# Optimization experiments

Hardware: AMD Instinct MI355X
Metric: run time of the kernel (lower is better)

Reference implementation:

```python
import jax, jax.numpy as jnp
import numpy as np

B, N, D, H, DK, DV, R = 4, 256, 256, 8, 32, 32, 64
EPS = 1e-6


def setup_inputs() -> dict:
    key = jax.random.key(0)
    ks = jax.random.split(key, 16)
    s = D ** -0.5
    return {
        "q": jax.random.normal(ks[0], (B, N, D), jnp.float32),
        "k": jax.random.normal(ks[1], (B, N, D), jnp.float32),
        "v": jax.random.normal(ks[2], (B, N, D), jnp.float32),
        "mask": jax.random.randint(ks[3], (B, N, N), 0, 2).astype(jnp.int32),
        "link": jax.random.uniform(ks[4], (B, N, N, R), jnp.float32),
        "Wq": jax.random.normal(ks[5], (D, H * DK), jnp.float32) * s,
        "Wk": jax.random.normal(ks[6], (D, H * DK), jnp.float32) * s,
        "Wr": jax.random.normal(ks[7], (D, H * DK), jnp.float32) * s,
        "Wv": jax.random.normal(ks[8], (D, H * DV), jnp.float32) * s,
        "Wvv": jax.random.normal(ks[9], (D, H * DV), jnp.float32) * s,
        "relationE": jax.random.normal(ks[10], (R, D), jnp.float32) * s,
        "Wo": jax.random.normal(ks[11], (H * DV, D), jnp.float32) * s,
        "gamma": jnp.ones((D,), jnp.float32),
        "beta": jnp.zeros((D,), jnp.float32),
    }


def reference(q, k, v, mask, link, Wq, Wk, Wr, Wv, Wvv, relationE, Wo, gamma, beta):
    # rela_num != 0 branch of Ruleformer MultiHeadAttention (dropout = identity, eval mode).
    residual = q
    b, n, d = q.shape
    # per-head projections of X (== q == residual in this branch): [b,h,n,dk]
    Xq = (q @ Wq).reshape(b, n, H, DK).transpose(0, 2, 1, 3)
    Xk = (q @ Wk).reshape(b, n, H, DK).transpose(0, 2, 1, 3)
    Xv = (q @ Wv).reshape(b, n, H, DV).transpose(0, 2, 1, 3)

    # calcE: relation-biased scores. Rk[b,i,j,h,d] = (link @ relationE @ Wr)
    Rk = jnp.einsum('bijr,re->bije', link, relationE @ Wr).reshape(b, n, n, H, DK)
    # attn[b,h,i,j] = Xq[b,h,i] . (Xk[b,h,j] + Rk[b,i,j,h])
    attn = jnp.einsum('bhid,bhjd->bhij', Xq, Xk)
    attn = attn + jnp.einsum('bijhd,bhid->bhij', Rk, Xq)
    attn = attn / (DK ** 0.5)
    attn = jnp.where(mask[:, None, :, :] == 0, -1e9, attn)
    alpha = jax.nn.softmax(attn, axis=-1)  # [b,h,n,n]

    # calcZ: Z[b,h,i] = sum_j alpha[b,h,i,j] * (Xv[b,h,j] + Rv[b,i,j,h])
    Rv = jnp.einsum('bijr,re->bije', link, relationE @ Wvv).reshape(b, n, n, H, DV)
    Z = jnp.einsum('bhij,bhjd->bhid', alpha, Xv)
    Z = Z + jnp.einsum('bhij,bijhd->bhid', alpha, Rv)

    out = Z.transpose(0, 2, 1, 3).reshape(b, n, H * DV) @ Wo
    out = out + residual
    mu = out.mean(-1, keepdims=True)
    var = ((out - mu) ** 2).mean(-1, keepdims=True)
    out = (out - mu) * jax.lax.rsqrt(var + EPS) * gamma + beta
    return out, alpha
```

## Files before the change

kernel.cpp:

```cpp
#include <hip/hip_runtime.h>
#include <math.h>

constexpr int B_ = 4, N_ = 256, D_ = 256, H_ = 8, DK_ = 32, DV_ = 32, R_ = 64;
constexpr float SCALE_ = 0.17677669529663687f;
constexpr float EPS_ = 1e-6f;

__global__ __launch_bounds__(256) void projekev_kernel(
        const float* __restrict__ q, const float* __restrict__ Wq,
        const float* __restrict__ Wk, const float* __restrict__ Wv,
        const float* __restrict__ relE, const float* __restrict__ Wr,
        const float* __restrict__ Wvv, float* __restrict__ Xq,
        float* __restrict__ Xk, float* __restrict__ Xv,
        float* __restrict__ Ek, float* __restrict__ Ev) {
    int blk = blockIdx.x;
    int t = threadIdx.x;
    __shared__ __align__(16) float ash[32 * 65];
    __shared__ __align__(16) float bsh[32 * 64];
    const float *src, *W;
    int rowbase, cbase, ct;
    float* dstE = nullptr;
    if (blk < 192) {
        ct = blk >> 4;
        int rt = blk & 15;
        src = q; rowbase = rt * 64;
        if (ct < 4)      { W = Wq; cbase = ct * 64; }
        else if (ct < 8) { W = Wk; cbase = (ct - 4) * 64; }
        else             { W = Wv; cbase = (ct - 8) * 64; }
    } else {
        int e = blk - 192;
        src = relE; rowbase = 0; ct = -1;
        W = (e < 4) ? Wr : Wvv;
        dstE = (e < 4) ? Ek : Ev;
        cbase = (e & 3) * 64;
    }
    int ti = t >> 4, tj = t & 15;
    float acc[4][4] = {{0.f}};
    for (int kc = 0; kc < 8; ++kc) {
        __syncthreads();
#pragma unroll
        for (int kk = 0; kk < 2; ++kk) {
            int m = t + kk * 256;
            int i = m >> 3, kq = m & 7;
            float4 v = *(const float4*)(src + (size_t)(rowbase + i) * 256 + kc * 32 + kq * 4);
            ash[(kq * 4 + 0) * 65 + i] = v.x;
            ash[(kq * 4 + 1) * 65 + i] = v.y;
            ash[(kq * 4 + 2) * 65 + i] = v.z;
            ash[(kq * 4 + 3) * 65 + i] = v.w;
        }
#pragma unroll
        for (int kk = 0; kk < 2; ++kk) {
            int m = t + kk * 256;
            int k = m >> 4, j4 = m & 15;
            float4 v = *(const float4*)(W + (size_t)(kc * 32 + k) * 256 + cbase + j4 * 4);
            *(float4*)(bsh + k * 64 + j4 * 4) = v;
        }
        __syncthreads();
#pragma unroll 8
        for (int k = 0; k < 32; ++k) {
            float4 av = *(const float4*)(ash + k * 65 + ti * 4);
            float4 bv = *(const float4*)(bsh + k * 64 + tj * 4);
            acc[0][0] += av.x * bv.x; acc[0][1] += av.x * bv.y;
            acc[0][2] += av.x * bv.z; acc[0][3] += av.x * bv.w;
            acc[1][0] += av.y * bv.x; acc[1][1] += av.y * bv.y;
            acc[1][2] += av.y * bv.z; acc[1][3] += av.y * bv.w;
            acc[2][0] += av.z * bv.x; acc[2][1] += av.z * bv.y;
            acc[2][2] += av.z * bv.z; acc[2][3] += av.z * bv.w;
            acc[3][0] += av.w * bv.x; acc[3][1] += av.w * bv.y;
            acc[3][2] += av.w * bv.z; acc[3][3] += av.w * bv.w;
        }
    }
    if (dstE) {
#pragma unroll
        for (int a = 0; a < 4; ++a) {
            int row = ti * 4 + a;
            *(float4*)(dstE + (size_t)row * 256 + cbase + tj * 4) =
                make_float4(acc[a][0], acc[a][1], acc[a][2], acc[a][3]);
        }
    } else {
        float* dst = (ct < 4) ? Xq : (ct < 8) ? Xk : Xv;
        int gcol = (ct & 3) * 64 + tj * 4;
        int h = gcol >> 5, dk = gcol & 31;
#pragma unroll
        for (int a = 0; a < 4; ++a) {
            int row = rowbase + ti * 4 + a;
            int bb = row >> 8, n = row & 255;
            *(float4*)(dst + ((size_t)(bb * 8 + h) * 256 + n) * 32 + dk) =
                make_float4(acc[a][0], acc[a][1], acc[a][2], acc[a][3]);
        }
    }
}

__global__ __launch_bounds__(256) void qkT_kernel(
        const float* __restrict__ Xq, const float* __restrict__ Xk,
        const float* __restrict__ Ek, float* __restrict__ qk,
        float* __restrict__ T) {
    int x = blockIdx.x;
    int t = threadIdx.x;
    __shared__ __align__(16) float xqsh[32 * 64];
    __shared__ __align__(16) float bsh2[32 * 64];
    bool isT = (x >= 512);
    int jt, it, bh;
    if (!isT) { jt = x & 3; it = (x >> 2) & 3; bh = x >> 4; }
    else      { int e = x - 512; jt = 0; it = e & 3; bh = e >> 2; }
    int b = bh >> 3, h = bh & 7;
#pragma unroll
    for (int k = 0; k < 2; ++k) {
        int m = t + k * 256;
        int i = m >> 3, dq4 = m & 7;
        float4 v = *(const float4*)(Xq + ((size_t)(bh * 256 + it * 64 + i)) * 32 + dq4 * 4);
        xqsh[(dq4 * 4 + 0) * 64 + i] = v.x;
        xqsh[(dq4 * 4 + 1) * 64 + i] = v.y;
        xqsh[(dq4 * 4 + 2) * 64 + i] = v.z;
        xqsh[(dq4 * 4 + 3) * 64 + i] = v.w;
    }
    if (!isT) {
#pragma unroll
        for (int k = 0; k < 2; ++k) {
            int m = t + k * 256;
            int i = m >> 3, dq4 = m & 7;
            float4 u = *(const float4*)(Xk + ((size_t)(bh * 256 + jt * 64 + i)) * 32 + dq4 * 4);
            bsh2[(dq4 * 4 + 0) * 64 + i] = u.x;
            bsh2[(dq4 * 4 + 1) * 64 + i] = u.y;
            bsh2[(dq4 * 4 + 2) * 64 + i] = u.z;
            bsh2[(dq4 * 4 + 3) * 64 + i] = u.w;
        }
    } else {
        int r = t >> 2, dq = t & 3;
#pragma unroll
        for (int kk = 0; kk < 2; ++kk) {
            int dq4 = dq + kk * 4;
            float4 v = *(const float4*)(Ek + r * 256 + h * 32 + dq4 * 4);
            bsh2[(dq4 * 4 + 0) * 64 + r] = v.x;
            bsh2[(dq4 * 4 + 1) * 64 + r] = v.y;
            bsh2[(dq4 * 4 + 2) * 64 + r] = v.z;
            bsh2[(dq4 * 4 + 3) * 64 + r] = v.w;
        }
    }
    __syncthreads();
    int ti = t >> 4, tj = t & 15;
    float acc[4][4] = {{0.f}};
#pragma unroll 8
    for (int dk = 0; dk < 32; ++dk) {
        float4 av = *(const float4*)(xqsh + dk * 64 + ti * 4);
        float4 bv = *(const float4*)(bsh2 + dk * 64 + tj * 4);
        acc[0][0] += av.x * bv.x; acc[0][1] += av.x * bv.y;
        acc[0][2] += av.x * bv.z; acc[0][3] += av.x * bv.w;
        acc[1][0] += av.y * bv.x; acc[1][1] += av.y * bv.y;
        acc[1][2] += av.y * bv.z; acc[1][3] += av.y * bv.w;
        acc[2][0] += av.z * bv.x; acc[2][1] += av.z * bv.y;
        acc[2][2] += av.z * bv.z; acc[2][3] += av.z * bv.w;
        acc[3][0] += av.w * bv.x; acc[3][1] += av.w * bv.y;
        acc[3][2] += av.w * bv.z; acc[3][3] += av.w * bv.w;
    }
    if (!isT) {
#pragma unroll
        for (int a = 0; a < 4; ++a) {
            int i = it * 64 + ti * 4 + a;
            *(float4*)(qk + ((size_t)(bh * 256 + i)) * 256 + jt * 64 + tj * 4) =
                make_float4(acc[a][0], acc[a][1], acc[a][2], acc[a][3]);
        }
    } else {
#pragma unroll
        for (int a = 0; a < 4; ++a) {
            int i = it * 64 + ti * 4 + a;
            *(float4*)(T + ((size_t)(b * 256 + i)) * 512 + h * 64 + tj * 4) =
                make_float4(acc[a][0], acc[a][1], acc[a][2], acc[a][3]);
        }
    }
}

__global__ __launch_bounds__(256) void expsz_kernel(
        const float* __restrict__ link, const float* __restrict__ Tg,
        const float* __restrict__ qk, const int* __restrict__ mask,
        const float* __restrict__ Xv, float* __restrict__ alphaU,
        float* __restrict__ Spart, float* __restrict__ Zpart,
        float* __restrict__ esumP) {
    int v = ((blockIdx.x & 7) << 9) | (blockIdx.x >> 3);
    int bi = v >> 2, jc = v & 3;
    int b = bi >> 8, i = bi & 255;
    int t = threadIdx.x;
    int g = t >> 6, jl = t & 63;
    int j0 = jc * 64;
    int h0 = g * 2, h1 = g * 2 + 1;

    __shared__ __align__(16) float linksh[64 * 68];
    __shared__ __align__(16) float Tsh[8 * 68];
    __shared__ __align__(16) float expsh[8 * 66];
    __shared__ __align__(16) float4 zsh[4 * 64];

    {
        const float4* lp4 = (const float4*)(link + ((size_t)bi * 256 + j0) * 64);
#pragma unroll
        for (int k = 0; k < 4; ++k) {
            int m = t + k * 256;
            int j = m >> 4, rq = m & 15;
            *(float4*)(linksh + j * 68 + rq * 4) = lp4[m];
        }
    }
    for (int m = t; m < 512; m += 256)
        Tsh[(m >> 6) * 68 + (m & 63)] = Tg[(size_t)bi * 512 + m];
    float qv0 = qk[((size_t)(b * 8 + h0) * 256 + i) * 256 + j0 + jl];
    float qv1 = qk[((size_t)(b * 8 + h1) * 256 + i) * 256 + j0 + jl];
    int mv = mask[((size_t)(b * 256 + i)) * 256 + j0 + jl];
    __syncthreads();

    float s0 = 0.f, s1 = 0.f;
    {
        const float4* lr = (const float4*)(linksh + jl * 68);
        const float4* t0 = (const float4*)(Tsh + h0 * 68);
        const float4* t1 = (const float4*)(Tsh + h1 * 68);
#pragma unroll
        for (int rq = 0; rq < 16; ++rq) {
            float4 lv = lr[rq];
            float4 a0 = t0[rq], a1 = t1[rq];
            s0 += lv.x * a0.x + lv.y * a0.y + lv.z * a0.z + lv.w * a0.w;
            s1 += lv.x * a1.x + lv.y * a1.y + lv.z * a1.z + lv.w * a1.w;
        }
    }
    s0 = (qv0 + s0) * SCALE_;
    s1 = (qv1 + s1) * SCALE_;
    if (mv == 0) { s0 = -1e9f; s1 = -1e9f; }
    float e0 = __expf(s0), e1 = __expf(s1);
    expsh[h0 * 66 + jl] = e0;
    expsh[h1 * 66 + jl] = e1;
    alphaU[((size_t)(b * 8 + h0) * 256 + i) * 256 + j0 + jl] = e0;
    alphaU[((size_t)(b * 8 + h1) * 256 + i) * 256 + j0 + jl] = e1;
    {
        float v0 = e0, v1 = e1;
        for (int off = 32; off > 0; off >>= 1) {
            v0 += __shfl_xor(v0, off);
            v1 += __shfl_xor(v1, off);
        }
        if (jl == 0) {
            esumP[((size_t)bi * 4 + jc) * 8 + h0] = v0;
            esumP[((size_t)bi * 4 + jc) * 8 + h1] = v1;
        }
    }
    __syncthreads();

    {
        float acc0 = 0.f, acc1 = 0.f;
        const float* ls = linksh + jl;
        const float* e0p = expsh + h0 * 66;
        const float* e1p = expsh + h1 * 66;
#pragma unroll 8
        for (int j = 0; j < 64; ++j) {
            float lv = ls[j * 68];
            acc0 += e0p[j] * lv;
            acc1 += e1p[j] * lv;
        }
        float* sp = Spart + ((size_t)bi * 4 + jc) * 512;
        sp[h0 * 64 + jl] = acc0;
        sp[h1 * 64 + jl] = acc1;
    }

    {
        int o = jl;
        int h = o >> 3, dv4 = o & 7;
        const float4* xv4 = (const float4*)Xv +
            (((size_t)(b * 8 + h)) * 256 + j0 + g * 16) * 8 + dv4;
        const float* ep = expsh + h * 66 + g * 16;
        float4 z = make_float4(0.f, 0.f, 0.f, 0.f);
#pragma unroll
        for (int j = 0; j < 16; ++j) {
            float a = ep[j];
            float4 x = xv4[j * 8];
            z.x += a * x.x; z.y += a * x.y; z.z += a * x.z; z.w += a * x.w;
        }
        zsh[g * 64 + o] = z;
    }
    __syncthreads();
    if (t < 64) {
        float4 z0 = zsh[t], z1 = zsh[64 + t], z2 = zsh[128 + t], z3 = zsh[192 + t];
        float4 z = make_float4(z0.x + z1.x + z2.x + z3.x,
                               z0.y + z1.y + z2.y + z3.y,
                               z0.z + z1.z + z2.z + z3.z,
                               z0.w + z1.w + z2.w + z3.w);
        *(float4*)(Zpart + ((size_t)bi * 4 + jc) * 256 + t * 4) = z;
    }
}

__global__ __launch_bounds__(256) void finout_kernel(
        const float* __restrict__ Spart, const float* __restrict__ Zpart,
        const float* __restrict__ esumP, const float* __restrict__ Ev,
        const float* __restrict__ Wo, const float* __restrict__ q,
        const float* __restrict__ gamma, const float* __restrict__ beta,
        float* __restrict__ alpha, float* __restrict__ out) {
    int row0 = blockIdx.x * 2;
    int b = row0 >> 8;
    int t = threadIdx.x;
    int lane = t & 63, wv = t >> 6;
    __shared__ __align__(16) float Ssh[8 * 68];
    __shared__ __align__(16) float zsh[512];
    __shared__ float invsh[16];
    __shared__ float redsh[16];

    for (int rr = 0; rr < 2; ++rr) {
        int row = row0 + rr;
        int i = row & 255;
        __syncthreads();
        if (t < 8) {
            float es = esumP[((size_t)row * 4 + 0) * 8 + t] +
                       esumP[((size_t)row * 4 + 1) * 8 + t] +
                       esumP[((size_t)row * 4 + 2) * 8 + t] +
                       esumP[((size_t)row * 4 + 3) * 8 + t];
            invsh[rr * 8 + t] = 1.f / es;
        }
        for (int m = t; m < 512; m += 256) {
            float sv = Spart[((size_t)row * 4 + 0) * 512 + m] +
                       Spart[((size_t)row * 4 + 1) * 512 + m] +
                       Spart[((size_t)row * 4 + 2) * 512 + m] +
                       Spart[((size_t)row * 4 + 3) * 512 + m];
            Ssh[(m >> 6) * 68 + (m & 63)] = sv;
        }
        __syncthreads();
#pragma unroll
        for (int k = 0; k < 8; ++k) {
            size_t off = ((size_t)(b * 8 + k) * 256 + i) * 256 + t;
            alpha[off] *= invsh[rr * 8 + k];
        }
        {
            int h = t >> 5, dv = t & 31;
            float zq = Zpart[((size_t)row * 4 + 0) * 256 + t] +
                       Zpart[((size_t)row * 4 + 1) * 256 + t] +
                       Zpart[((size_t)row * 4 + 2) * 256 + t] +
                       Zpart[((size_t)row * 4 + 3) * 256 + t];
            float acc = 0.f;
            const float* sp = Ssh + h * 68;
            const float* evp = Ev + h * 32 + dv;
#pragma unroll 4
            for (int r = 0; r < 64; ++r) acc += sp[r] * evp[r * 256];
            zsh[rr * 256 + t] = (zq + acc) * invsh[rr * 8 + h];
        }
    }
    __syncthreads();

    float a0 = q[(size_t)row0 * 256 + t];
    float a1 = q[(size_t)(row0 + 1) * 256 + t];
    for (int d4 = 0; d4 < 64; ++d4) {
        float w0 = Wo[(d4 * 4 + 0) * 256 + t];
        float w1 = Wo[(d4 * 4 + 1) * 256 + t];
        float w2 = Wo[(d4 * 4 + 2) * 256 + t];
        float w3 = Wo[(d4 * 4 + 3) * 256 + t];
        float4 z0v = *(const float4*)(zsh + d4 * 4);
        float4 z1v = *(const float4*)(zsh + 256 + d4 * 4);
        a0 += z0v.x * w0 + z0v.y * w1 + z0v.z * w2 + z0v.w * w3;
        a1 += z1v.x * w0 + z1v.y * w1 + z1v.z * w2 + z1v.w * w3;
    }
    float acc2[2] = {a0, a1};
#pragma unroll
    for (int rr = 0; rr < 2; ++rr) {
        float v = acc2[rr], v2 = acc2[rr] * acc2[rr];
        for (int off = 32; off > 0; off >>= 1) {
            v += __shfl_xor(v, off);
            v2 += __shfl_xor(v2, off);
        }
        if (lane == 0) {
            redsh[rr * 8 + wv] = v;
            redsh[rr * 8 + 4 + wv] = v2;
        }
    }
    __syncthreads();
#pragma unroll
    for (int rr = 0; rr < 2; ++rr) {
        float sum = redsh[rr * 8 + 0] + redsh[rr * 8 + 1] + redsh[rr * 8 + 2] + redsh[rr * 8 + 3];
        float sum2 = redsh[rr * 8 + 4] + redsh[rr * 8 + 5] + redsh[rr * 8 + 6] + redsh[rr * 8 + 7];
        float mu = sum * (1.f / 256.f);
        float var = sum2 * (1.f / 256.f) - mu * mu;
        float dev = acc2[rr] - mu;
        out[(size_t)(row0 + rr) * 256 + t] = dev * rsqrtf(var + EPS_) * gamma[t] + beta[t];
    }
}

extern "C" void kernel_launch(void* const* d_in, const int* in_sizes, int n_in,
                              void* d_out, int out_size, void* d_ws, size_t ws_size,
                              hipStream_t stream) {
    const float* q     = (const float*)d_in[0];
    const int*   mask  = (const int*)d_in[3];
    const float* link  = (const float*)d_in[4];
    const float* Wq    = (const float*)d_in[5];
    const float* Wk    = (const float*)d_in[6];
    const float* Wr    = (const float*)d_in[7];
    const float* Wv    = (const float*)d_in[8];
    const float* Wvv   = (const float*)d_in[9];
    const float* relE  = (const float*)d_in[10];
    const float* Wo    = (const float*)d_in[11];
    const float* gamma = (const float*)d_in[12];
    const float* beta  = (const float*)d_in[13];

    float* out   = (float*)d_out;
    float* alpha = out + B_ * N_ * D_;

    float* ws = (float*)d_ws;
    float* Ek    = ws;
    float* Ev    = Ek + 16384;
    float* Xq    = Ev + 16384;
    float* Xk    = Xq + 262144;
    float* Xv    = Xk + 262144;
    float* T     = Xv + 262144;
    float* qkbuf = T + 524288;
    float* Spart = qkbuf + 2097152;
    float* Zpart = Spart + 2097152;
    float* esumP = Zpart + 1048576;

    projekev_kernel<<<200, 256, 0, stream>>>(q, Wq, Wk, Wv, relE, Wr, Wvv,
                                             Xq, Xk, Xv, Ek, Ev);
    qkT_kernel<<<640, 256, 0, stream>>>(Xq, Xk, Ek, qkbuf, T);
    expsz_kernel<<<4096, 256, 0, stream>>>(link, T, qkbuf, mask, Xv,
                                           alpha, Spart, Zpart, esumP);
    finout_kernel<<<512, 256, 0, stream>>>(Spart, Zpart, esumP, Ev, Wo, q,
                                           gamma, beta, alpha, out);
}
```

Before: 183.7 us.

## Fuse finalize into exp/Z kernel with last-block-done atomic counter

Merges the final normalization, output projection and layernorm into the exp/Z kernel. Each row's four j-chunk blocks bump an atomic counter, and the last one to arrive does the row finalization. The relation-value term is now applied per chunk inside the block by multiplying by Ev, which removes the large Spart buffer and its global write and read. The aim is to save a kernel launch and that intermediate traffic, at the cost of a memset, extra per-block Ev reads, and a serialized tail on the last-arriving blocks.

```diff
diff --git a/kernel.cpp b/kernel.cpp
--- a/kernel.cpp
+++ b/kernel.cpp
@@ -169,12 +169,15 @@
     }
 }
 
-__global__ __launch_bounds__(256) void expsz_kernel(
+__global__ __launch_bounds__(256) void expszfin_kernel(
         const float* __restrict__ link, const float* __restrict__ Tg,
         const float* __restrict__ qk, const int* __restrict__ mask,
-        const float* __restrict__ Xv, float* __restrict__ alphaU,
-        float* __restrict__ Spart, float* __restrict__ Zpart,
-        float* __restrict__ esumP) {
+        const float* __restrict__ Xv, const float* __restrict__ Ev,
+        const float* __restrict__ Wo, const float* __restrict__ q,
+        const float* __restrict__ gamma, const float* __restrict__ beta,
+        float* __restrict__ alpha, float* __restrict__ Zpart,
+        float* __restrict__ esumP, int* __restrict__ cnt,
+        float* __restrict__ out) {
     int v = ((blockIdx.x & 7) << 9) | (blockIdx.x >> 3);
     int bi = v >> 2, jc = v & 3;
     int b = bi >> 8, i = bi & 255;
@@ -186,7 +189,8 @@
     __shared__ __align__(16) float linksh[64 * 68];
     __shared__ __align__(16) float Tsh[8 * 68];
     __shared__ __align__(16) float expsh[8 * 66];
-    __shared__ __align__(16) float4 zsh[4 * 64];
+    __shared__ __align__(16) float zshf[4 * 264];
+    __shared__ int finflag;
 
     {
         const float4* lp4 = (const float4*)(link + ((size_t)bi * 256 + j0) * 64);
@@ -223,8 +227,8 @@
     float e0 = __expf(s0), e1 = __expf(s1);
     expsh[h0 * 66 + jl] = e0;
     expsh[h1 * 66 + jl] = e1;
-    alphaU[((size_t)(b * 8 + h0) * 256 + i) * 256 + j0 + jl] = e0;
-    alphaU[((size_t)(b * 8 + h1) * 256 + i) * 256 + j0 + jl] = e1;
+    alpha[((size_t)(b * 8 + h0) * 256 + i) * 256 + j0 + jl] = e0;
+    alpha[((size_t)(b * 8 + h1) * 256 + i) * 256 + j0 + jl] = e1;
     {
         float v0 = e0, v1 = e1;
         for (int off = 32; off > 0; off >>= 1) {
@@ -249,9 +253,16 @@
             acc0 += e0p[j] * lv;
             acc1 += e1p[j] * lv;
         }
-        float* sp = Spart + ((size_t)bi * 4 + jc) * 512;
-        sp[h0 * 64 + jl] = acc0;
-        sp[h1 * 64 + jl] = acc1;
+        Tsh[h0 * 68 + jl] = acc0;
+        Tsh[h1 * 68 + jl] = acc1;
+    }
+
+    float zsev = 0.f;
+    {
+        const float* sp = Tsh + (t >> 5) * 68;
+        const float* evp = Ev + t;
+#pragma unroll 4
+        for (int r = 0; r < 64; ++r) zsev += sp[r] * evp[(size_t)r * 256];
     }
 
     {
@@ -267,108 +278,74 @@
             float4 x = xv4[j * 8];
             z.x += a * x.x; z.y += a * x.y; z.z += a * x.z; z.w += a * x.w;
         }
-        zsh[g * 64 + o] = z;
-    }
-    __syncthreads();
-    if (t < 64) {
-        float4 z0 = zsh[t], z1 = zsh[64 + t], z2 = zsh[128 + t], z3 = zsh[192 + t];
-        float4 z = make_float4(z0.x + z1.x + z2.x + z3.x,
-                               z0.y + z1.y + z2.y + z3.y,
-                               z0.z + z1.z + z2.z + z3.z,
-                               z0.w + z1.w + z2.w + z3.w);
-        *(float4*)(Zpart + ((size_t)bi * 4 + jc) * 256 + t * 4) = z;
-    }
-}
-
-__global__ __launch_bounds__(256) void finout_kernel(
-        const float* __restrict__ Spart, const float* __restrict__ Zpart,
-        const float* __restrict__ esumP, const float* __restrict__ Ev,
-        const float* __restrict__ Wo, const float* __restrict__ q,
-        const float* __restrict__ gamma, const float* __restrict__ beta,
-        float* __restrict__ alpha, float* __restrict__ out) {
-    int row0 = blockIdx.x * 2;
-    int b = row0 >> 8;
-    int t = threadIdx.x;
-    int lane = t & 63, wv = t >> 6;
-    __shared__ __align__(16) float Ssh[8 * 68];
-    __shared__ __align__(16) float zsh[512];
-    __shared__ float invsh[16];
-    __shared__ float redsh[16];
-
-    for (int rr = 0; rr < 2; ++rr) {
-        int row = row0 + rr;
-        int i = row & 255;
-        __syncthreads();
-        if (t < 8) {
-            float es = esumP[((size_t)row * 4 + 0) * 8 + t] +
-                       esumP[((size_t)row * 4 + 1) * 8 + t] +
-                       esumP[((size_t)row * 4 + 2) * 8 + t] +
-                       esumP[((size_t)row * 4 + 3) * 8 + t];
-            invsh[rr * 8 + t] = 1.f / es;
-        }
-        for (int m = t; m < 512; m += 256) {
-            float sv = Spart[((size_t)row * 4 + 0) * 512 + m] +
-                       Spart[((size_t)row * 4 + 1) * 512 + m] +
-                       Spart[((size_t)row * 4 + 2) * 512 + m] +
-                       Spart[((size_t)row * 4 + 3) * 512 + m];
-            Ssh[(m >> 6) * 68 + (m & 63)] = sv;
-        }
-        __syncthreads();
-#pragma unroll
-        for (int k = 0; k < 8; ++k) {
-            size_t off = ((size_t)(b * 8 + k) * 256 + i) * 256 + t;
-            alpha[off] *= invsh[rr * 8 + k];
-        }
-        {
-            int h = t >> 5, dv = t & 31;
-            float zq = Zpart[((size_t)row * 4 + 0) * 256 + t] +
-                       Zpart[((size_t)row * 4 + 1) * 256 + t] +
-                       Zpart[((size_t)row * 4 + 2) * 256 + t] +
-                       Zpart[((size_t)row * 4 + 3) * 256 + t];
-            float acc = 0.f;
-            const float* sp = Ssh + h * 68;
-            const float* evp = Ev + h * 32 + dv;
+        *(float4*)(zshf + g * 264 + o * 4) = z;
+    }
+    __syncthreads();
+    {
+        float zq = zsev + zshf[t] + zshf[264 + t] + zshf[528 + t] + zshf[792 + t];
+        Zpart[((size_t)bi * 4 + jc) * 256 + t] = zq;
+    }
+
+    __threadfence();
+    __syncthreads();
+    if (t == 0) {
+        int old = atomicAdd(cnt + bi, 1);
+        finflag = (old == 3) ? 1 : 0;
+    }
+    __syncthreads();
+    if (!finflag) return;
+    __threadfence();
+
+    float* zrow = linksh;
+    float* invl = linksh + 256;
+    float* redl = linksh + 272;
+    if (t < 8) {
+        float es = esumP[((size_t)bi * 4 + 0) * 8 + t] +
+                   esumP[((size_t)bi * 4 + 1) * 8 + t] +
+                   esumP[((size_t)bi * 4 + 2) * 8 + t] +
+                   esumP[((size_t)bi * 4 + 3) * 8 + t];
+        invl[t] = 1.f / es;
+    }
+    __syncthreads();
+    {
+        float zq = Zpart[((size_t)bi * 4 + 0) * 256 + t] +
+                   Zpart[((size_t)bi * 4 + 1) * 256 + t] +
+                   Zpart[((size_t)bi * 4 + 2) * 256 + t] +
+                   Zpart[((size_t)bi * 4 + 3) * 256 + t];
+        zrow[t] = zq * invl[t >> 5];
+    }
+#pragma unroll
+    for (int k = 0; k < 8; ++k) {
+        size_t off = ((size_t)(b * 8 + k) * 256 + i) * 256 + t;
+        alpha[off] *= invl[k];
+    }
+    __syncthreads();
+    float a = q[(size_t)bi * 256 + t];
+    {
+        const float4* z4 = (const float4*)zrow;
+        const float* wp = Wo + t;
 #pragma unroll 4
-            for (int r = 0; r < 64; ++r) acc += sp[r] * evp[r * 256];
-            zsh[rr * 256 + t] = (zq + acc) * invsh[rr * 8 + h];
-        }
-    }
-    __syncthreads();
-
-    float a0 = q[(size_t)row0 * 256 + t];
-    float a1 = q[(size_t)(row0 + 1) * 256 + t];
-    for (int d4 = 0; d4 < 64; ++d4) {
-        float w0 = Wo[(d4 * 4 + 0) * 256 + t];
-        float w1 = Wo[(d4 * 4 + 1) * 256 + t];
-        float w2 = Wo[(d4 * 4 + 2) * 256 + t];
-        float w3 = Wo[(d4 * 4 + 3) * 256 + t];
-        float4 z0v = *(const float4*)(zsh + d4 * 4);
-        float4 z1v = *(const float4*)(zsh + 256 + d4 * 4);
-        a0 += z0v.x * w0 + z0v.y * w1 + z0v.z * w2 + z0v.w * w3;
-        a1 += z1v.x * w0 + z1v.y * w1 + z1v.z * w2 + z1v.w * w3;
-    }
-    float acc2[2] = {a0, a1};
-#pragma unroll
-    for (int rr = 0; rr < 2; ++rr) {
-        float v = acc2[rr], v2 = acc2[rr] * acc2[rr];
+        for (int d4 = 0; d4 < 64; ++d4) {
+            float4 zz = z4[d4];
+            a += zz.x * wp[(d4 * 4 + 0) * 256] + zz.y * wp[(d4 * 4 + 1) * 256] +
+                 zz.z * wp[(d4 * 4 + 2) * 256] + zz.w * wp[(d4 * 4 + 3) * 256];
+        }
+    }
+    {
+        float v2 = a, vq = a * a;
         for (int off = 32; off > 0; off >>= 1) {
-            v += __shfl_xor(v, off);
             v2 += __shfl_xor(v2, off);
-        }
-        if (lane == 0) {
-            redsh[rr * 8 + wv] = v;
-            redsh[rr * 8 + 4 + wv] = v2;
-        }
-    }
-    __syncthreads();
-#pragma unroll
-    for (int rr = 0; rr < 2; ++rr) {
-        float sum = redsh[rr * 8 + 0] + redsh[rr * 8 + 1] + redsh[rr * 8 + 2] + redsh[rr * 8 + 3];
-        float sum2 = redsh[rr * 8 + 4] + redsh[rr * 8 + 5] + redsh[rr * 8 + 6] + redsh[rr * 8 + 7];
+            vq += __shfl_xor(vq, off);
+        }
+        if (jl == 0) { redl[g] = v2; redl[8 + g] = vq; }
+    }
+    __syncthreads();
+    {
+        float sum = redl[0] + redl[1] + redl[2] + redl[3];
+        float sum2 = redl[8] + redl[9] + redl[10] + redl[11];
         float mu = sum * (1.f / 256.f);
         float var = sum2 * (1.f / 256.f) - mu * mu;
-        float dev = acc2[rr] - mu;
-        out[(size_t)(row0 + rr) * 256 + t] = dev * rsqrtf(var + EPS_) * gamma[t] + beta[t];
+        out[(size_t)bi * 256 + t] = (a - mu) * rsqrtf(var + EPS_) * gamma[t] + beta[t];
     }
 }
 
@@ -399,15 +376,15 @@
     float* Xv    = Xk + 262144;
     float* T     = Xv + 262144;
     float* qkbuf = T + 524288;
-    float* Spart = qkbuf + 2097152;
-    float* Zpart = Spart + 2097152;
+    float* Zpart = qkbuf + 2097152;
     float* esumP = Zpart + 1048576;
-
+    int*   cnt   = (int*)(esumP + 32768);
+
+    hipMemsetAsync(cnt, 0, 1024 * sizeof(int), stream);
     projekev_kernel<<<200, 256, 0, stream>>>(q, Wq, Wk, Wv, relE, Wr, Wvv,
                                              Xq, Xk, Xv, Ek, Ev);
     qkT_kernel<<<640, 256, 0, stream>>>(Xq, Xk, Ek, qkbuf, T);
-    expsz_kernel<<<4096, 256, 0, stream>>>(link, T, qkbuf, mask, Xv,
-                                           alpha, Spart, Zpart, esumP);
-    finout_kernel<<<512, 256, 0, stream>>>(Spart, Zpart, esumP, Ev, Wo, q,
-                                           gamma, beta, alpha, out);
+    expszfin_kernel<<<4096, 256, 0, stream>>>(link, T, qkbuf, mask, Xv, Ev,
+                                              Wo, q, gamma, beta, alpha,
+                                              Zpart, esumP, cnt, out);
 }
```

Result: slower. 710.4 us (+286.8%).

## Fold relation-value contraction into expsz kernel and drop Spart buffer

Applied to the files above, without the earlier changes.

Each expsz block now contracts its per-chunk exp-weighted link sums with Ev, and adds the Xv term itself, before writing Zpart. This removes the large Spart intermediate, which was written to global memory and re-read by finout, along with the Ev matmul there. In exchange each of the 4096 blocks does an extra 64-step reduction over Ev through L2 and uses scalar Xv loads. It also drops several barriers, relying on each wave only touching its own heads' shared rows.

```diff
diff --git a/kernel.cpp b/kernel.cpp
--- a/kernel.cpp
+++ b/kernel.cpp
@@ -172,8 +172,8 @@
 __global__ __launch_bounds__(256) void expsz_kernel(
         const float* __restrict__ link, const float* __restrict__ Tg,
         const float* __restrict__ qk, const int* __restrict__ mask,
-        const float* __restrict__ Xv, float* __restrict__ alphaU,
-        float* __restrict__ Spart, float* __restrict__ Zpart,
+        const float* __restrict__ Xv, const float* __restrict__ Ev,
+        float* __restrict__ alphaU, float* __restrict__ Zpart,
         float* __restrict__ esumP) {
     int v = ((blockIdx.x & 7) << 9) | (blockIdx.x >> 3);
     int bi = v >> 2, jc = v & 3;
@@ -186,7 +186,6 @@
     __shared__ __align__(16) float linksh[64 * 68];
     __shared__ __align__(16) float Tsh[8 * 68];
     __shared__ __align__(16) float expsh[8 * 66];
-    __shared__ __align__(16) float4 zsh[4 * 64];
 
     {
         const float4* lp4 = (const float4*)(link + ((size_t)bi * 256 + j0) * 64);
@@ -236,7 +235,6 @@
             esumP[((size_t)bi * 4 + jc) * 8 + h1] = v1;
         }
     }
-    __syncthreads();
 
     {
         float acc0 = 0.f, acc1 = 0.f;
@@ -249,40 +247,27 @@
             acc0 += e0p[j] * lv;
             acc1 += e1p[j] * lv;
         }
-        float* sp = Spart + ((size_t)bi * 4 + jc) * 512;
-        sp[h0 * 64 + jl] = acc0;
-        sp[h1 * 64 + jl] = acc1;
-    }
-
-    {
-        int o = jl;
-        int h = o >> 3, dv4 = o & 7;
-        const float4* xv4 = (const float4*)Xv +
-            (((size_t)(b * 8 + h)) * 256 + j0 + g * 16) * 8 + dv4;
-        const float* ep = expsh + h * 66 + g * 16;
-        float4 z = make_float4(0.f, 0.f, 0.f, 0.f);
-#pragma unroll
-        for (int j = 0; j < 16; ++j) {
-            float a = ep[j];
-            float4 x = xv4[j * 8];
-            z.x += a * x.x; z.y += a * x.y; z.z += a * x.z; z.w += a * x.w;
-        }
-        zsh[g * 64 + o] = z;
-    }
-    __syncthreads();
-    if (t < 64) {
-        float4 z0 = zsh[t], z1 = zsh[64 + t], z2 = zsh[128 + t], z3 = zsh[192 + t];
-        float4 z = make_float4(z0.x + z1.x + z2.x + z3.x,
-                               z0.y + z1.y + z2.y + z3.y,
-                               z0.z + z1.z + z2.z + z3.z,
-                               z0.w + z1.w + z2.w + z3.w);
-        *(float4*)(Zpart + ((size_t)bi * 4 + jc) * 256 + t * 4) = z;
+        Tsh[h0 * 68 + jl] = acc0;
+        Tsh[h1 * 68 + jl] = acc1;
+    }
+
+    {
+        int h = t >> 5, dv = t & 31;
+        float z = 0.f;
+        const float* sp = Tsh + h * 68;
+        const float* evp = Ev + t;
+#pragma unroll 4
+        for (int r = 0; r < 64; ++r) z += sp[r] * evp[(size_t)r * 256];
+        const float* ep = expsh + h * 66;
+        const float* xvp = Xv + (((size_t)(b * 8 + h)) * 256 + j0) * 32 + dv;
+#pragma unroll 8
+        for (int j = 0; j < 64; ++j) z += ep[j] * xvp[j * 32];
+        Zpart[((size_t)bi * 4 + jc) * 256 + t] = z;
     }
 }
 
 __global__ __launch_bounds__(256) void finout_kernel(
-        const float* __restrict__ Spart, const float* __restrict__ Zpart,
-        const float* __restrict__ esumP, const float* __restrict__ Ev,
+        const float* __restrict__ Zpart, const float* __restrict__ esumP,
         const float* __restrict__ Wo, const float* __restrict__ q,
         const float* __restrict__ gamma, const float* __restrict__ beta,
         float* __restrict__ alpha, float* __restrict__ out) {
@@ -290,15 +275,14 @@
     int b = row0 >> 8;
     int t = threadIdx.x;
     int lane = t & 63, wv = t >> 6;
-    __shared__ __align__(16) float Ssh[8 * 68];
     __shared__ __align__(16) float zsh[512];
     __shared__ float invsh[16];
     __shared__ float redsh[16];
 
+#pragma unroll
     for (int rr = 0; rr < 2; ++rr) {
         int row = row0 + rr;
         int i = row & 255;
-        __syncthreads();
         if (t < 8) {
             float es = esumP[((size_t)row * 4 + 0) * 8 + t] +
                        esumP[((size_t)row * 4 + 1) * 8 + t] +
@@ -306,31 +290,18 @@
                        esumP[((size_t)row * 4 + 3) * 8 + t];
             invsh[rr * 8 + t] = 1.f / es;
         }
-        for (int m = t; m < 512; m += 256) {
-            float sv = Spart[((size_t)row * 4 + 0) * 512 + m] +
-                       Spart[((size_t)row * 4 + 1) * 512 + m] +
-                       Spart[((size_t)row * 4 + 2) * 512 + m] +
-                       Spart[((size_t)row * 4 + 3) * 512 + m];
-            Ssh[(m >> 6) * 68 + (m & 63)] = sv;
-        }
         __syncthreads();
-#pragma unroll
-        for (int k = 0; k < 8; ++k) {
-            size_t off = ((size_t)(b * 8 + k) * 256 + i) * 256 + t;
-            alpha[off] *= invsh[rr * 8 + k];
-        }
         {
-            int h = t >> 5, dv = t & 31;
             float zq = Zpart[((size_t)row * 4 + 0) * 256 + t] +
                        Zpart[((size_t)row * 4 + 1) * 256 + t] +
                        Zpart[((size_t)row * 4 + 2) * 256 + t] +
                        Zpart[((size_t)row * 4 + 3) * 256 + t];
-            float acc = 0.f;
-            const float* sp = Ssh + h * 68;
-            const float* evp = Ev + h * 32 + dv;
-#pragma unroll 4
-            for (int r = 0; r < 64; ++r) acc += sp[r] * evp[r * 256];
-            zsh[rr * 256 + t] = (zq + acc) * invsh[rr * 8 + h];
+            zsh[rr * 256 + t] = zq * invsh[rr * 8 + (t >> 5)];
+        }
+#pragma unroll
+        for (int k = 0; k < 8; ++k) {
+            size_t off = ((size_t)(b * 8 + k) * 256 + i) * 256 + t;
+            alpha[off] *= invsh[rr * 8 + k];
         }
     }
     __syncthreads();
@@ -399,15 +370,14 @@
     float* Xv    = Xk + 262144;
     float* T     = Xv + 262144;
     float* qkbuf = T + 524288;
-    float* Spart = qkbuf + 2097152;
-    float* Zpart = Spart + 2097152;
+    float* Zpart = qkbuf + 2097152;
     float* esumP = Zpart + 1048576;
 
     projekev_kernel<<<200, 256, 0, stream>>>(q, Wq, Wk, Wv, relE, Wr, Wvv,
                                              Xq, Xk, Xv, Ek, Ev);
     qkT_kernel<<<640, 256, 0, stream>>>(Xq, Xk, Ek, qkbuf, T);
-    expsz_kernel<<<4096, 256, 0, stream>>>(link, T, qkbuf, mask, Xv,
-                                           alpha, Spart, Zpart, esumP);
-    finout_kernel<<<512, 256, 0, stream>>>(Spart, Zpart, esumP, Ev, Wo, q,
+    expsz_kernel<<<4096, 256, 0, stream>>>(link, T, qkbuf, mask, Xv, Ev,
+                                           alpha, Zpart, esumP);
+    finout_kernel<<<512, 256, 0, stream>>>(Zpart, esumP, Wo, q,
                                            gamma, beta, alpha, out);
 }
```

Result: slower. 188.6 us (+2.7%).
